# Kernel tuning notes

Measured on AMD Instinct MI355X. Metric: run time of the kernel, lower is better.

## Reference

```python
import jax, jax.numpy as jnp
import numpy as np

N = 50000      # nodes
E = 800000     # edges (before self loops)
D_IN = 64      # input atom feature dim
HID = 128      # hidden_dim
HEADS = 4
C = HID // HEADS  # 32 per-head channels
ED = 12        # edge feature dim
L = 4          # num GAT layers
EPS = 1e-5


def setup_inputs() -> dict:
    key = jax.random.key(0)
    ks = jax.random.split(key, 10)
    s = 0.1
    return {
        "x": jax.random.normal(ks[0], (N, D_IN), jnp.float32),
        "edge_index": jax.random.randint(ks[1], (2, E), 0, N, dtype=jnp.int32),
        "edge_attr": jax.random.uniform(ks[2], (E, ED), jnp.float32),
        "Wp": jax.random.normal(ks[3], (D_IN, HID), jnp.float32) * s,
        "bp": jnp.zeros((HID,), jnp.float32),
        "W": jax.random.normal(ks[4], (L, HID, HID), jnp.float32) * s,
        "We": jax.random.normal(ks[5], (L, ED, HID), jnp.float32) * s,
        "att_src": jax.random.normal(ks[6], (L, HEADS, C), jnp.float32) * s,
        "att_dst": jax.random.normal(ks[7], (L, HEADS, C), jnp.float32) * s,
        "att_edge": jax.random.normal(ks[8], (L, HEADS, C), jnp.float32) * s,
        "bias": jnp.zeros((L, HID), jnp.float32),
        "gamma": jnp.ones((L, HID), jnp.float32),
        "beta": jnp.zeros((L, HID), jnp.float32),
    }


def _gat_layer(h, src, dst, ea_full, W, We, a_s, a_d, a_e, b):
    # PyG GATConv: x' = x W -> [N, heads, C]; attention uses edge features, msg = alpha * x'_src
    xp = (h @ W).reshape(N, HEADS, C)
    e_emb = (ea_full @ We).reshape(-1, HEADS, C)          # [E', heads, C]
    a_src = (xp * a_s).sum(-1)                            # [N, heads]
    a_dst = (xp * a_d).sum(-1)
    a = a_src[src] + a_dst[dst] + (e_emb * a_e).sum(-1)   # [E', heads]
    a = jax.nn.leaky_relu(a, 0.2)
    # segment softmax over destination node neighborhoods
    amax = jax.ops.segment_max(a, dst, num_segments=N)
    ex = jnp.exp(a - amax[dst])
    denom = jax.ops.segment_sum(ex, dst, num_segments=N)
    alpha = ex / denom[dst]                               # [E', heads]
    msg = alpha[:, :, None] * xp[src]                     # [E', heads, C]
    out = jax.ops.segment_sum(msg, dst, num_segments=N)   # [N, heads, C]
    return out.reshape(N, HID) + b


def reference(x, edge_index, edge_attr, Wp, bp, W, We, att_src, att_dst, att_edge, bias, gamma, beta):
    # PyG GATConv add_self_loops=True with fill_value='mean' for edge_attr
    loop = jnp.arange(N, dtype=edge_index.dtype)
    src = jnp.concatenate([edge_index[0], loop])
    dst = jnp.concatenate([edge_index[1], loop])
    ea_mean = edge_attr.mean(0)
    ea_full = jnp.concatenate([edge_attr, jnp.broadcast_to(ea_mean, (N, ED))], 0)

    h = jax.nn.relu(x @ Wp + bp)
    for i in range(L):
        h_in = h
        h = _gat_layer(h, src, dst, ea_full, W[i], We[i], att_src[i], att_dst[i], att_edge[i], bias[i])
        # BatchNorm1d (training-mode batch statistics)
        mu = h.mean(0)
        var = ((h - mu) ** 2).mean(0)
        h = gamma[i] * (h - mu) / jnp.sqrt(var + EPS) + beta[i]
        h = jax.nn.relu(h)
        if i > 0:
            h = h + h_in
    return h
```

## Files before the change

kernel.cpp:

```cpp
#include <hip/hip_runtime.h>

constexpr int N_NODES = 50000;
constexpr int N_EDGES = 800000;
constexpr int N_ETOT  = N_EDGES + N_NODES;
constexpr int HID     = 128;
constexpr int HEADS   = 4;
constexpr int ED      = 12;
constexpr int LAYERS  = 4;
constexpr float BN_EPS = 1e-5f;
constexpr int SCAN_BLK = (N_NODES + 255) / 256;
constexpr int EB = (N_ETOT + 255) / 256;
constexpr int GB = (N_NODES + 63) / 64;
constexpr int WB = (LAYERS * HID * HID + 255) / 256;

typedef __attribute__((ext_vector_type(8))) short short8;
typedef __attribute__((ext_vector_type(4))) float floatx4;

__device__ inline unsigned bf16pair(float a, float b) {
    unsigned ua = __float_as_uint(a), ub = __float_as_uint(b);
    ua = (ua + 0x7FFFu + ((ua >> 16) & 1u)) >> 16;
    ub = (ub + 0x7FFFu + ((ub >> 16) & 1u)) >> 16;
    return ua | (ub << 16);
}

__launch_bounds__(256)
__global__ void pre1_kernel(const int* __restrict__ dst, int* __restrict__ hist,
                            int* __restrict__ rank,
                            const float* __restrict__ ea, float* __restrict__ easum,
                            const float* __restrict__ W, unsigned short* __restrict__ wb) {
    __shared__ float ls[12];
    int bid = blockIdx.x, t = threadIdx.x;
    if (bid < EB) {
        int e = bid * 256 + t;
        if (e < N_ETOT) {
            int d = (e < N_EDGES) ? dst[e] : (e - N_EDGES);
            rank[e] = atomicAdd(&hist[d], 1);
        }
    } else if (bid < EB + 256) {
        int b2 = bid - EB;
        if (t < 12) ls[t] = 0.f;
        __syncthreads();
        float loc[12];
#pragma unroll
        for (int d = 0; d < 12; d++) loc[d] = 0.f;
        for (int e = b2 * 256 + t; e < N_EDGES; e += 256 * 256) {
            const float* er = ea + (size_t)e * ED;
#pragma unroll
            for (int d = 0; d < 12; d++) loc[d] += er[d];
        }
#pragma unroll
        for (int d = 0; d < 12; d++) atomicAdd(&ls[d], loc[d]);
        __syncthreads();
        if (t < 12) atomicAdd(&easum[t], ls[t]);
    } else {
        int idx = (bid - EB - 256) * 256 + t;
        if (idx < LAYERS * HID * HID) {
            int l = idx >> 14;
            int k = (idx >> 7) & 127;
            int n = idx & 127;
            unsigned u = __float_as_uint(W[idx]);
            u = (u + 0x7FFFu + ((u >> 16) & 1u)) >> 16;
            int kt = k >> 5, q = (k & 31) >> 3, j = k & 7;
            int nt = n >> 4, c = n & 15;
            int lane = q * 16 + c;
            wb[(size_t)l * 16384 + ((size_t)(kt * 8 + nt) * 64 + lane) * 8 + j] =
                (unsigned short)u;
        }
    }
}

__global__ void blocksum_kernel(const int* __restrict__ hist, int* __restrict__ bsum) {
    __shared__ int sd[256];
    int t = threadIdx.x;
    int n = blockIdx.x * 256 + t;
    sd[t] = (n < N_NODES) ? hist[n] : 0;
    __syncthreads();
#pragma unroll
    for (int off = 128; off; off >>= 1) {
        if (t < off) sd[t] += sd[t + off];
        __syncthreads();
    }
    if (t == 0) bsum[blockIdx.x] = sd[0];
}

__launch_bounds__(256)
__global__ void pre2_kernel(const int* __restrict__ bsum, int* __restrict__ boff,
                            int* __restrict__ rowp, const float* __restrict__ easum,
                            const float* __restrict__ We, const float* __restrict__ att_edge,
                            float* __restrict__ wea_all, float* __restrict__ aloop) {
    int t = threadIdx.x;
    if (blockIdx.x == 0) {
        __shared__ int sd[256];
        int v = (t < SCAN_BLK) ? bsum[t] : 0;
        sd[t] = v;
        __syncthreads();
#pragma unroll
        for (int off = 1; off < 256; off <<= 1) {
            int u = (t >= off) ? sd[t - off] : 0;
            __syncthreads();
            sd[t] += u;
            __syncthreads();
        }
        if (t < SCAN_BLK) boff[t] = sd[t] - v;
        if (t == 255) rowp[N_NODES] = sd[255];
    } else {
        __shared__ float em[12];
        __shared__ float weash[LAYERS * ED * HEADS];
        if (t < 12) em[t] = easum[t] / (float)N_EDGES;
        if (t < LAYERS * ED * HEADS) {
            int l = t / (ED * HEADS);
            int r = t % (ED * HEADS);
            int d = r / HEADS;
            int h = r % HEADS;
            float sum = 0.f;
#pragma unroll
            for (int c = 0; c < 32; c++)
                sum += We[((size_t)(l * ED + d)) * HID + h * 32 + c] *
                       att_edge[(l * HEADS + h) * 32 + c];
            wea_all[t] = sum;
            weash[t] = sum;
        }
        __syncthreads();
        if (t < LAYERS * HEADS) {
            int l = t / HEADS, h = t % HEADS;
            float s = 0.f;
#pragma unroll
            for (int d = 0; d < 12; d++) s += em[d] * weash[l * ED * HEADS + d * HEADS + h];
            aloop[t] = s;
        }
    }
}

__global__ void rowp_kernel(const int* __restrict__ hist, const int* __restrict__ boff,
                            int* __restrict__ rowp) {
    __shared__ int sd[256];
    int t = threadIdx.x;
    int n = blockIdx.x * 256 + t;
    int v = (n < N_NODES) ? hist[n] : 0;
    sd[t] = v;
    __syncthreads();
#pragma unroll
    for (int off = 1; off < 256; off <<= 1) {
        int u = (t >= off) ? sd[t - off] : 0;
        __syncthreads();
        sd[t] += u;
        __syncthreads();
    }
    if (n < N_NODES) {
        int excl = sd[t] - v + boff[blockIdx.x];
        rowp[n] = excl;
    }
}

__launch_bounds__(256)
__global__ void pre3_kernel(const int* __restrict__ src, const int* __restrict__ dst,
                            const int* __restrict__ rank, const int* __restrict__ rowp,
                            int2* __restrict__ csr,
                            const float* __restrict__ A, const float* __restrict__ B,
                            const float* __restrict__ bias, float* __restrict__ C,
                            unsigned* __restrict__ Cb) {
    __shared__ float Bs[64 * 128];
    int t = threadIdx.x;
    if (blockIdx.x < EB) {
        int e = blockIdx.x * 256 + t;
        if (e >= N_ETOT) return;
        int s, d;
        if (e < N_EDGES) { s = src[e]; d = dst[e]; }
        else             { s = d = e - N_EDGES; }
        int pos = rowp[d] + rank[e];
        csr[pos] = make_int2(s, e);
        return;
    }
    constexpr int K = 64;
    int bid = blockIdx.x - EB;
    const float4* B4 = (const float4*)B;
    float4* Bs4 = (float4*)Bs;
#pragma unroll
    for (int i = t; i < K * 32; i += 256) Bs4[i] = B4[i];
    __syncthreads();

    int c0 = (t & 15) * 8;
    int r0 = (t >> 4) * 4;
    int rbase = bid * 64 + r0;

    float acc[4][8];
#pragma unroll
    for (int j = 0; j < 4; j++)
#pragma unroll
        for (int c = 0; c < 8; c++) acc[j][c] = 0.f;

    const float4* A4 = (const float4*)A;
    int rg[4];
#pragma unroll
    for (int j = 0; j < 4; j++) rg[j] = min(rbase + j, N_NODES - 1);

    for (int kk = 0; kk < K; kk += 4) {
        float4 av[4];
#pragma unroll
        for (int j = 0; j < 4; j++) av[j] = A4[(size_t)rg[j] * (K / 4) + (kk >> 2)];
        float a_arr[4][4];
#pragma unroll
        for (int j = 0; j < 4; j++) {
            a_arr[j][0] = av[j].x; a_arr[j][1] = av[j].y;
            a_arr[j][2] = av[j].z; a_arr[j][3] = av[j].w;
        }
#pragma unroll
        for (int jj = 0; jj < 4; jj++) {
            float4 b0 = Bs4[(kk + jj) * 32 + (c0 >> 2)];
            float4 b1 = Bs4[(kk + jj) * 32 + (c0 >> 2) + 1];
#pragma unroll
            for (int j = 0; j < 4; j++) {
                float a = a_arr[j][jj];
                acc[j][0] += a * b0.x; acc[j][1] += a * b0.y;
                acc[j][2] += a * b0.z; acc[j][3] += a * b0.w;
                acc[j][4] += a * b1.x; acc[j][5] += a * b1.y;
                acc[j][6] += a * b1.z; acc[j][7] += a * b1.w;
            }
        }
    }

#pragma unroll
    for (int j = 0; j < 4; j++) {
        int r = rbase + j;
        if (r < N_NODES) {
            float o[8];
#pragma unroll
            for (int c = 0; c < 8; c++) o[c] = fmaxf(acc[j][c] + bias[c0 + c], 0.f);
            ((float4*)(C + (size_t)r * 128 + c0))[0] = make_float4(o[0], o[1], o[2], o[3]);
            ((float4*)(C + (size_t)r * 128 + c0 + 4))[0] = make_float4(o[4], o[5], o[6], o[7]);
            uint4 pk;
            pk.x = bf16pair(o[0], o[1]); pk.y = bf16pair(o[2], o[3]);
            pk.z = bf16pair(o[4], o[5]); pk.w = bf16pair(o[6], o[7]);
            ((uint4*)(Cb + (size_t)r * 64 + (c0 >> 1)))[0] = pk;
        }
    }
}

__launch_bounds__(256)
__global__ void pre4_kernel(const int2* __restrict__ csr, const float* __restrict__ ea,
                            const float* __restrict__ wea_all, const float* __restrict__ aloop,
                            uint2* __restrict__ aecsr,
                            const unsigned short* __restrict__ hAb,
                            const unsigned short* __restrict__ wb,
                            const float* __restrict__ att_s, const float* __restrict__ att_d,
                            unsigned* __restrict__ xpb,
                            float* __restrict__ asrc, float* __restrict__ adst) {
    __shared__ float smem[4 * 16 * 129];
    int t = threadIdx.x;
    if (blockIdx.x < EB) {
        float* wsh = smem;
        float* lsh = smem + 192;
        if (t < LAYERS * ED * HEADS) wsh[t] = wea_all[t];
        if (t < LAYERS * HEADS) lsh[t] = aloop[t];
        __syncthreads();
        int i = blockIdx.x * 256 + t;
        if (i >= N_ETOT) return;
        int e = csr[i].y;
        float a[LAYERS][4];
        if (e < N_EDGES) {
            float er[12];
            const float* ep = ea + (size_t)e * ED;
#pragma unroll
            for (int d = 0; d < 12; d++) er[d] = ep[d];
#pragma unroll
            for (int l = 0; l < LAYERS; l++)
#pragma unroll
                for (int h = 0; h < 4; h++) {
                    float s = 0.f;
#pragma unroll
                    for (int d = 0; d < 12; d++) s += er[d] * wsh[l * 48 + d * 4 + h];
                    a[l][h] = s;
                }
        } else {
#pragma unroll
            for (int l = 0; l < LAYERS; l++)
#pragma unroll
                for (int h = 0; h < 4; h++) a[l][h] = lsh[l * 4 + h];
        }
#pragma unroll
        for (int l = 0; l < LAYERS; l++)
            aecsr[(size_t)l * N_ETOT + i] =
                make_uint2(bf16pair(a[l][0], a[l][1]), bf16pair(a[l][2], a[l][3]));
        return;
    }
    int bid = blockIdx.x - EB;
    float (*lds)[16][129] = (float (*)[16][129])smem;
    int w = t >> 6, lane = t & 63;
    int rbase = bid * 64 + w * 16;
    int mrow = lane & 15, quad = lane >> 4;

    floatx4 acc[8];
#pragma unroll
    for (int nt = 0; nt < 8; nt++) acc[nt] = (floatx4){0.f, 0.f, 0.f, 0.f};

    int arow = min(rbase + mrow, N_NODES - 1);
    const short8* wb8 = (const short8*)wb;
#pragma unroll
    for (int kt = 0; kt < 4; kt++) {
        short8 afrag = *(const short8*)(hAb + (size_t)arow * 128 + kt * 32 + quad * 8);
#pragma unroll
        for (int nt = 0; nt < 8; nt++) {
            short8 bfrag = wb8[(kt * 8 + nt) * 64 + lane];
            acc[nt] = __builtin_amdgcn_mfma_f32_16x16x32_bf16(afrag, bfrag, acc[nt], 0, 0, 0);
        }
    }
#pragma unroll
    for (int nt = 0; nt < 8; nt++)
#pragma unroll
        for (int rr = 0; rr < 4; rr++)
            lds[w][quad * 4 + rr][nt * 16 + mrow] = acc[nt][rr];

    int row = lane >> 2, h = lane & 3;
    int r = rbase + row;
    float vals[32];
    float ps = 0.f, pd = 0.f;
#pragma unroll
    for (int c = 0; c < 32; c++) {
        float v = lds[w][row][h * 32 + c];
        vals[c] = v;
        ps += v * att_s[h * 32 + c];
        pd += v * att_d[h * 32 + c];
    }
    if (r < N_NODES) {
        unsigned* dstp = xpb + (size_t)r * 64 + h * 16;
#pragma unroll
        for (int qq = 0; qq < 4; qq++) {
            uint4 o;
            o.x = bf16pair(vals[qq * 8 + 0], vals[qq * 8 + 1]);
            o.y = bf16pair(vals[qq * 8 + 2], vals[qq * 8 + 3]);
            o.z = bf16pair(vals[qq * 8 + 4], vals[qq * 8 + 5]);
            o.w = bf16pair(vals[qq * 8 + 6], vals[qq * 8 + 7]);
            ((uint4*)dstp)[qq] = o;
        }
        asrc[r * 4 + h] = ps;
        adst[r * 4 + h] = pd;
    }
}

template <int ADD>
__launch_bounds__(256)
__global__ void gemm_fused_kernel(const float* __restrict__ outb,
                                  const float* __restrict__ bnsum,
                                  const float* __restrict__ bnsum2,
                                  const float* __restrict__ gamma,
                                  const float* __restrict__ beta,
                                  float* __restrict__ hA,
                                  const unsigned short* __restrict__ wb,
                                  const float* __restrict__ att_s,
                                  const float* __restrict__ att_d,
                                  unsigned* __restrict__ xpb,
                                  float* __restrict__ asrc, float* __restrict__ adst) {
    __shared__ float lds[4][16][129];
    __shared__ float sc_s[128], sh_s[128];
    int t = threadIdx.x;
    if (t < 128) {
        float mu = bnsum[t] / (float)N_NODES;
        float var = bnsum2[t] / (float)N_NODES - mu * mu;
        float inv = rsqrtf(var + BN_EPS);
        float g = gamma[t] * inv;
        sc_s[t] = g;
        sh_s[t] = beta[t] - mu * g;
    }
    __syncthreads();

    int w = t >> 6, lane = t & 63;
    int rbase = blockIdx.x * 64 + w * 16;
    int mrow = lane & 15, quad = lane >> 4;
    int arow = rbase + mrow;
    bool owner = arow < N_NODES;
    int ar = min(arow, N_NODES - 1);

    floatx4 acc[8];
#pragma unroll
    for (int nt = 0; nt < 8; nt++) acc[nt] = (floatx4){0.f, 0.f, 0.f, 0.f};

    const short8* wb8 = (const short8*)wb;
#pragma unroll
    for (int kt = 0; kt < 4; kt++) {
        int cb = kt * 32 + quad * 8;
        const float4* ob = (const float4*)(outb + (size_t)ar * 128 + cb);
        float4 o0 = ob[0], o1 = ob[1];
        float v[8];
        v[0] = fmaxf(o0.x * sc_s[cb + 0] + sh_s[cb + 0], 0.f);
        v[1] = fmaxf(o0.y * sc_s[cb + 1] + sh_s[cb + 1], 0.f);
        v[2] = fmaxf(o0.z * sc_s[cb + 2] + sh_s[cb + 2], 0.f);
        v[3] = fmaxf(o0.w * sc_s[cb + 3] + sh_s[cb + 3], 0.f);
        v[4] = fmaxf(o1.x * sc_s[cb + 4] + sh_s[cb + 4], 0.f);
        v[5] = fmaxf(o1.y * sc_s[cb + 5] + sh_s[cb + 5], 0.f);
        v[6] = fmaxf(o1.z * sc_s[cb + 6] + sh_s[cb + 6], 0.f);
        v[7] = fmaxf(o1.w * sc_s[cb + 7] + sh_s[cb + 7], 0.f);
        if (ADD) {
            const float4* hp = (const float4*)(hA + (size_t)ar * 128 + cb);
            float4 h0 = hp[0], h1 = hp[1];
            v[0] += h0.x; v[1] += h0.y; v[2] += h0.z; v[3] += h0.w;
            v[4] += h1.x; v[5] += h1.y; v[6] += h1.z; v[7] += h1.w;
        }
        if (owner) {
            float4* hw = (float4*)(hA + (size_t)ar * 128 + cb);
            hw[0] = make_float4(v[0], v[1], v[2], v[3]);
            hw[1] = make_float4(v[4], v[5], v[6], v[7]);
        }
        uint4 pk;
        pk.x = bf16pair(v[0], v[1]); pk.y = bf16pair(v[2], v[3]);
        pk.z = bf16pair(v[4], v[5]); pk.w = bf16pair(v[6], v[7]);
        short8 afrag = *(short8*)&pk;
#pragma unroll
        for (int nt = 0; nt < 8; nt++) {
            short8 bfrag = wb8[(kt * 8 + nt) * 64 + lane];
            acc[nt] = __builtin_amdgcn_mfma_f32_16x16x32_bf16(afrag, bfrag, acc[nt], 0, 0, 0);
        }
    }

#pragma unroll
    for (int nt = 0; nt < 8; nt++)
#pragma unroll
        for (int rr = 0; rr < 4; rr++)
            lds[w][quad * 4 + rr][nt * 16 + mrow] = acc[nt][rr];

    int row = lane >> 2, h = lane & 3;
    int r = rbase + row;
    float vals[32];
    float ps = 0.f, pd = 0.f;
#pragma unroll
    for (int c = 0; c < 32; c++) {
        float v = lds[w][row][h * 32 + c];
        vals[c] = v;
        ps += v * att_s[h * 32 + c];
        pd += v * att_d[h * 32 + c];
    }
    if (r < N_NODES) {
        unsigned* dstp = xpb + (size_t)r * 64 + h * 16;
#pragma unroll
        for (int qq = 0; qq < 4; qq++) {
            uint4 o;
            o.x = bf16pair(vals[qq * 8 + 0], vals[qq * 8 + 1]);
            o.y = bf16pair(vals[qq * 8 + 2], vals[qq * 8 + 3]);
            o.z = bf16pair(vals[qq * 8 + 4], vals[qq * 8 + 5]);
            o.w = bf16pair(vals[qq * 8 + 6], vals[qq * 8 + 7]);
            ((uint4*)dstp)[qq] = o;
        }
        asrc[r * 4 + h] = ps;
        adst[r * 4 + h] = pd;
    }
}

__launch_bounds__(256)
__global__ void node_kernel(const uint2* __restrict__ aecsr, const float* __restrict__ asrc,
                            const float* __restrict__ adst, const int* __restrict__ rowp,
                            const int2* __restrict__ csr, const unsigned* __restrict__ xpb,
                            float* __restrict__ out) {
    int gw = (blockIdx.x * blockDim.x + threadIdx.x) >> 6;
    int lane = threadIdx.x & 63;
    if (gw >= N_NODES) return;
    int sub = lane >> 4;
    int sl  = lane & 15;
    int h   = sl >> 2;
    int beg = rowp[gw], end = rowp[gw + 1];
    const uint4* xp4 = (const uint4*)xpb;
    float adh = adst[gw * 4 + h];

    float a[8];
#pragma unroll
    for (int c = 0; c < 8; c++) a[c] = 0.f;
    float den = 0.f;

#define PROC(JJ)                                                                 \
    {                                                                            \
        int2 se = csr[JJ];                                                       \
        uint2 ae = aecsr[JJ];                                                    \
        unsigned aw = (h & 2) ? ae.y : ae.x;                                     \
        float aeh = __uint_as_float((h & 1) ? (aw & 0xFFFF0000u) : (aw << 16));  \
        float ash = asrc[se.x * 4 + h];                                          \
        uint4 v = xp4[(size_t)se.x * 16 + sl];                                   \
        float lg = ash + adh + aeh;                                              \
        lg = (lg > 0.f) ? lg : 0.2f * lg;                                        \
        float ex = __expf(fminf(lg, 60.f));                                      \
        a[0] += ex * __uint_as_float(v.x << 16);                                 \
        a[1] += ex * __uint_as_float(v.x & 0xFFFF0000u);                         \
        a[2] += ex * __uint_as_float(v.y << 16);                                 \
        a[3] += ex * __uint_as_float(v.y & 0xFFFF0000u);                         \
        a[4] += ex * __uint_as_float(v.z << 16);                                 \
        a[5] += ex * __uint_as_float(v.z & 0xFFFF0000u);                         \
        a[6] += ex * __uint_as_float(v.w << 16);                                 \
        a[7] += ex * __uint_as_float(v.w & 0xFFFF0000u);                         \
        den += ex;                                                               \
    }

    int j = beg + sub;
    for (; j + 12 < end; j += 16) {
        PROC(j); PROC(j + 4); PROC(j + 8); PROC(j + 12);
    }
    for (; j < end; j += 4) PROC(j);
#undef PROC

#pragma unroll
    for (int c = 0; c < 8; c++) {
        a[c] += __shfl_xor(a[c], 16);
        a[c] += __shfl_xor(a[c], 32);
    }
    den += __shfl_xor(den, 16);
    den += __shfl_xor(den, 32);
    float inv = 1.0f / den;
    if (sub == 0) {
        float* op = out + (size_t)gw * 128 + sl * 8;
        ((float4*)op)[0] = make_float4(a[0] * inv, a[1] * inv, a[2] * inv, a[3] * inv);
        ((float4*)op)[1] = make_float4(a[4] * inv, a[5] * inv, a[6] * inv, a[7] * inv);
    }
}

__launch_bounds__(256)
__global__ void bnstats_kernel(const float* __restrict__ h, float* __restrict__ bnsum,
                               float* __restrict__ bnsum2) {
    __shared__ float ls[256], ls2[256];
    int t = threadIdx.x;
    int c = t & 127, half = t >> 7;
    int r0 = blockIdx.x * 128;
    float s = 0.f, s2 = 0.f;
    int rend = min(r0 + 128, N_NODES);
    for (int r = r0 + half; r < rend; r += 2) {
        float v = h[(size_t)r * 128 + c];
        s += v; s2 += v * v;
    }
    ls[t] = s; ls2[t] = s2;
    __syncthreads();
    if (half == 0) {
        s += ls[t + 128]; s2 += ls2[t + 128];
        atomicAdd(&bnsum[c], s);
        atomicAdd(&bnsum2[c], s2);
    }
}

__launch_bounds__(256)
__global__ void finalupd_kernel(const float* __restrict__ outb, const float* __restrict__ bnsum,
                                const float* __restrict__ bnsum2, const float* __restrict__ gamma,
                                const float* __restrict__ beta, const float* __restrict__ hA,
                                float* __restrict__ dst) {
    __shared__ float sc_s[128], sh_s[128];
    int t = threadIdx.x;
    if (t < 128) {
        float mu = bnsum[t] / (float)N_NODES;
        float var = bnsum2[t] / (float)N_NODES - mu * mu;
        float inv = rsqrtf(var + BN_EPS);
        float g = gamma[t] * inv;
        sc_s[t] = g;
        sh_s[t] = beta[t] - mu * g;
    }
    __syncthreads();
    int i = blockIdx.x * blockDim.x + t;
    if (i >= N_NODES * 32) return;
    int c4 = (i & 31) * 4;
    float4 o = ((const float4*)outb)[i];
    float4 hh = ((const float4*)hA)[i];
    float4 v;
    v.x = fmaxf(o.x * sc_s[c4 + 0] + sh_s[c4 + 0], 0.f) + hh.x;
    v.y = fmaxf(o.y * sc_s[c4 + 1] + sh_s[c4 + 1], 0.f) + hh.y;
    v.z = fmaxf(o.z * sc_s[c4 + 2] + sh_s[c4 + 2], 0.f) + hh.z;
    v.w = fmaxf(o.w * sc_s[c4 + 3] + sh_s[c4 + 3], 0.f) + hh.w;
    ((float4*)dst)[i] = v;
}

extern "C" void kernel_launch(void* const* d_in, const int* in_sizes, int n_in,
                              void* d_out, int out_size, void* d_ws, size_t ws_size,
                              hipStream_t stream) {
    const float* x          = (const float*)d_in[0];
    const int*   edge_index = (const int*)d_in[1];
    const float* edge_attr  = (const float*)d_in[2];
    const float* Wp         = (const float*)d_in[3];
    const float* bp         = (const float*)d_in[4];
    const float* W          = (const float*)d_in[5];
    const float* We         = (const float*)d_in[6];
    const float* att_src    = (const float*)d_in[7];
    const float* att_dst    = (const float*)d_in[8];
    const float* att_edge   = (const float*)d_in[9];
    const float* gamma      = (const float*)d_in[11];
    const float* beta       = (const float*)d_in[12];
    float* outp = (float*)d_out;

    const int* ei_src = edge_index;
    const int* ei_dst = edge_index + N_EDGES;

    char* p = (char*)d_ws;
    auto alloc = [&](size_t nbytes) {
        char* r = p;
        p += (nbytes + 255) & ~(size_t)255;
        return r;
    };
    int*   hist     = (int*)alloc((size_t)N_NODES * 4);
    float* easum    = (float*)alloc(16 * 4);
    float* bnsumall = (float*)alloc((size_t)LAYERS * 256 * 4);
    size_t zero_bytes = (char*)(bnsumall + LAYERS * 256) - (char*)hist;

    float* hA       = (float*)alloc((size_t)N_NODES * 128 * 4);
    unsigned* hAb   = (unsigned*)alloc((size_t)N_NODES * 64 * 4);
    unsigned* xpb   = (unsigned*)alloc((size_t)N_NODES * 64 * 4);
    float* outb     = (float*)alloc((size_t)N_NODES * 128 * 4);
    float* asrc     = (float*)alloc((size_t)N_NODES * 4 * 4);
    float* adst     = (float*)alloc((size_t)N_NODES * 4 * 4);
    float* wea_all  = (float*)alloc((LAYERS * 48 + 16) * 4);
    float* aloop    = wea_all + LAYERS * 48;
    unsigned short* wb = (unsigned short*)alloc((size_t)LAYERS * 16384 * 2);
    int* rowp       = (int*)alloc(((size_t)N_NODES + 1) * 4);
    int* rankbuf    = (int*)alloc((size_t)N_ETOT * 4);
    int2* csr       = (int2*)alloc((size_t)N_ETOT * 8);
    uint2* aecsr    = (uint2*)alloc((size_t)LAYERS * N_ETOT * 8);
    int* bsum       = (int*)alloc(256 * 4);
    int* boff       = (int*)alloc(256 * 4);

    (void)hipMemsetAsync(hist, 0, zero_bytes, stream);

    pre1_kernel<<<EB + 256 + WB, 256, 0, stream>>>(ei_dst, hist, rankbuf, edge_attr, easum, W, wb);
    blocksum_kernel<<<SCAN_BLK, 256, 0, stream>>>(hist, bsum);
    pre2_kernel<<<2, 256, 0, stream>>>(bsum, boff, rowp, easum, We, att_edge, wea_all, aloop);
    rowp_kernel<<<SCAN_BLK, 256, 0, stream>>>(hist, boff, rowp);
    pre3_kernel<<<EB + GB, 256, 0, stream>>>(ei_src, ei_dst, rankbuf, rowp, csr, x, Wp, bp, hA, hAb);
    pre4_kernel<<<EB + GB, 256, 0, stream>>>(csr, edge_attr, wea_all, aloop, aecsr,
                                             (const unsigned short*)hAb, wb,
                                             att_src, att_dst, xpb, asrc, adst);

    for (int l = 0; l < LAYERS; l++) {
        float* bnsum  = bnsumall + l * 256;
        float* bnsum2 = bnsum + 128;
        node_kernel<<<(N_NODES + 3) / 4, 256, 0, stream>>>(
            aecsr + (size_t)l * N_ETOT, asrc, adst, rowp, csr, xpb, outb);
        bnstats_kernel<<<(N_NODES + 127) / 128, 256, 0, stream>>>(outb, bnsum, bnsum2);
        if (l < LAYERS - 1) {
            if (l == 0)
                gemm_fused_kernel<0><<<GB, 256, 0, stream>>>(
                    outb, bnsum, bnsum2, gamma + l * 128, beta + l * 128, hA,
                    wb + (size_t)(l + 1) * 16384, att_src + (l + 1) * 128,
                    att_dst + (l + 1) * 128, xpb, asrc, adst);
            else
                gemm_fused_kernel<1><<<GB, 256, 0, stream>>>(
                    outb, bnsum, bnsum2, gamma + l * 128, beta + l * 128, hA,
                    wb + (size_t)(l + 1) * 16384, att_src + (l + 1) * 128,
                    att_dst + (l + 1) * 128, xpb, asrc, adst);
        } else {
            finalupd_kernel<<<(N_NODES * 32 + 255) / 256, 256, 0, stream>>>(
                outb, bnsum, bnsum2, gamma + l * 128, beta + l * 128, hA, outp);
        }
    }
}
```

Before: 615.7 us.

## Replicate degree histogram to cut atomic contention and regroup preprocessing kernels

```diff
diff --git a/kernel.cpp b/kernel.cpp
--- a/kernel.cpp
+++ b/kernel.cpp
@@ -8,7 +8,9 @@
 constexpr int ED      = 12;
 constexpr int LAYERS  = 4;
 constexpr float BN_EPS = 1e-5f;
-constexpr int SCAN_BLK = (N_NODES + 255) / 256;
+constexpr int R_REP = 4;
+constexpr int RN = N_NODES * R_REP;
+constexpr int SB2 = (RN + 255) / 256;
 constexpr int EB = (N_ETOT + 255) / 256;
 constexpr int GB = (N_NODES + 63) / 64;
 constexpr int WB = (LAYERS * HID * HID + 255) / 256;
@@ -24,20 +26,87 @@
 }
 
 __launch_bounds__(256)
-__global__ void pre1_kernel(const int* __restrict__ dst, int* __restrict__ hist,
+__global__ void pre1_kernel(const int* __restrict__ dst, int* __restrict__ hist2,
                             int* __restrict__ rank,
                             const float* __restrict__ ea, float* __restrict__ easum,
-                            const float* __restrict__ W, unsigned short* __restrict__ wb) {
-    __shared__ float ls[12];
+                            const float* __restrict__ W, unsigned short* __restrict__ wb,
+                            const float* __restrict__ A, const float* __restrict__ B,
+                            const float* __restrict__ bias, float* __restrict__ C,
+                            unsigned* __restrict__ Cb) {
+    __shared__ float smem[64 * 128];
     int bid = blockIdx.x, t = threadIdx.x;
-    if (bid < EB) {
-        int e = bid * 256 + t;
+    if (bid < GB) {
+        constexpr int K = 64;
+        const float4* B4 = (const float4*)B;
+        float4* Bs4 = (float4*)smem;
+#pragma unroll
+        for (int i = t; i < K * 32; i += 256) Bs4[i] = B4[i];
+        __syncthreads();
+
+        int c0 = (t & 15) * 8;
+        int r0 = (t >> 4) * 4;
+        int rbase = bid * 64 + r0;
+
+        float acc[4][8];
+#pragma unroll
+        for (int j = 0; j < 4; j++)
+#pragma unroll
+            for (int c = 0; c < 8; c++) acc[j][c] = 0.f;
+
+        const float4* A4 = (const float4*)A;
+        int rg[4];
+#pragma unroll
+        for (int j = 0; j < 4; j++) rg[j] = min(rbase + j, N_NODES - 1);
+
+        for (int kk = 0; kk < K; kk += 4) {
+            float4 av[4];
+#pragma unroll
+            for (int j = 0; j < 4; j++) av[j] = A4[(size_t)rg[j] * (K / 4) + (kk >> 2)];
+            float a_arr[4][4];
+#pragma unroll
+            for (int j = 0; j < 4; j++) {
+                a_arr[j][0] = av[j].x; a_arr[j][1] = av[j].y;
+                a_arr[j][2] = av[j].z; a_arr[j][3] = av[j].w;
+            }
+#pragma unroll
+            for (int jj = 0; jj < 4; jj++) {
+                float4 b0 = Bs4[(kk + jj) * 32 + (c0 >> 2)];
+                float4 b1 = Bs4[(kk + jj) * 32 + (c0 >> 2) + 1];
+#pragma unroll
+                for (int j = 0; j < 4; j++) {
+                    float a = a_arr[j][jj];
+                    acc[j][0] += a * b0.x; acc[j][1] += a * b0.y;
+                    acc[j][2] += a * b0.z; acc[j][3] += a * b0.w;
+                    acc[j][4] += a * b1.x; acc[j][5] += a * b1.y;
+                    acc[j][6] += a * b1.z; acc[j][7] += a * b1.w;
+                }
+            }
+        }
+
+#pragma unroll
+        for (int j = 0; j < 4; j++) {
+            int r = rbase + j;
+            if (r < N_NODES) {
+                float o[8];
+#pragma unroll
+                for (int c = 0; c < 8; c++) o[c] = fmaxf(acc[j][c] + bias[c0 + c], 0.f);
+                ((float4*)(C + (size_t)r * 128 + c0))[0] = make_float4(o[0], o[1], o[2], o[3]);
+                ((float4*)(C + (size_t)r * 128 + c0 + 4))[0] = make_float4(o[4], o[5], o[6], o[7]);
+                uint4 pk;
+                pk.x = bf16pair(o[0], o[1]); pk.y = bf16pair(o[2], o[3]);
+                pk.z = bf16pair(o[4], o[5]); pk.w = bf16pair(o[6], o[7]);
+                ((uint4*)(Cb + (size_t)r * 64 + (c0 >> 1)))[0] = pk;
+            }
+        }
+    } else if (bid < GB + EB) {
+        int e = (bid - GB) * 256 + t;
         if (e < N_ETOT) {
             int d = (e < N_EDGES) ? dst[e] : (e - N_EDGES);
-            rank[e] = atomicAdd(&hist[d], 1);
-        }
-    } else if (bid < EB + 256) {
-        int b2 = bid - EB;
+            rank[e] = atomicAdd(&hist2[(e & (R_REP - 1)) * N_NODES + d], 1);
+        }
+    } else if (bid < GB + EB + 256) {
+        int b2 = bid - GB - EB;
+        float* ls = smem;
         if (t < 12) ls[t] = 0.f;
         __syncthreads();
         float loc[12];
@@ -53,7 +122,7 @@
         __syncthreads();
         if (t < 12) atomicAdd(&easum[t], ls[t]);
     } else {
-        int idx = (bid - EB - 256) * 256 + t;
+        int idx = (bid - GB - EB - 256) * 256 + t;
         if (idx < LAYERS * HID * HID) {
             int l = idx >> 14;
             int k = (idx >> 7) & 127;
@@ -69,11 +138,13 @@
     }
 }
 
-__global__ void blocksum_kernel(const int* __restrict__ hist, int* __restrict__ bsum) {
+__global__ void blocksum_kernel(const int* __restrict__ hist2, int* __restrict__ bsum) {
     __shared__ int sd[256];
     int t = threadIdx.x;
-    int n = blockIdx.x * 256 + t;
-    sd[t] = (n < N_NODES) ? hist[n] : 0;
+    int f = blockIdx.x * 256 + t;
+    int v = 0;
+    if (f < RN) v = hist2[(f & (R_REP - 1)) * N_NODES + (f >> 2)];
+    sd[t] = v;
     __syncthreads();
 #pragma unroll
     for (int off = 128; off; off >>= 1) {
@@ -85,14 +156,19 @@
 
 __launch_bounds__(256)
 __global__ void pre2_kernel(const int* __restrict__ bsum, int* __restrict__ boff,
-                            int* __restrict__ rowp, const float* __restrict__ easum,
+                            int* __restrict__ rowpR, const float* __restrict__ easum,
                             const float* __restrict__ We, const float* __restrict__ att_edge,
                             float* __restrict__ wea_all, float* __restrict__ aloop) {
     int t = threadIdx.x;
     if (blockIdx.x == 0) {
         __shared__ int sd[256];
-        int v = (t < SCAN_BLK) ? bsum[t] : 0;
-        sd[t] = v;
+        int b = 4 * t;
+        int v0 = (b + 0 < SB2) ? bsum[b + 0] : 0;
+        int v1 = (b + 1 < SB2) ? bsum[b + 1] : 0;
+        int v2 = (b + 2 < SB2) ? bsum[b + 2] : 0;
+        int v3 = (b + 3 < SB2) ? bsum[b + 3] : 0;
+        int tot = v0 + v1 + v2 + v3;
+        sd[t] = tot;
         __syncthreads();
 #pragma unroll
         for (int off = 1; off < 256; off <<= 1) {
@@ -101,8 +177,12 @@
             sd[t] += u;
             __syncthreads();
         }
-        if (t < SCAN_BLK) boff[t] = sd[t] - v;
-        if (t == 255) rowp[N_NODES] = sd[255];
+        int excl = sd[t] - tot;
+        if (b + 0 < SB2) boff[b + 0] = excl;
+        if (b + 1 < SB2) boff[b + 1] = excl + v0;
+        if (b + 2 < SB2) boff[b + 2] = excl + v0 + v1;
+        if (b + 3 < SB2) boff[b + 3] = excl + v0 + v1 + v2;
+        if (t == 255) rowpR[RN] = sd[255];
     } else {
         __shared__ float em[12];
         __shared__ float weash[LAYERS * ED * HEADS];
@@ -131,12 +211,12 @@
     }
 }
 
-__global__ void rowp_kernel(const int* __restrict__ hist, const int* __restrict__ boff,
-                            int* __restrict__ rowp) {
+__global__ void rowp_kernel(const int* __restrict__ hist2, const int* __restrict__ boff,
+                            int* __restrict__ rowpR) {
     __shared__ int sd[256];
     int t = threadIdx.x;
-    int n = blockIdx.x * 256 + t;
-    int v = (n < N_NODES) ? hist[n] : 0;
+    int f = blockIdx.x * 256 + t;
+    int v = (f < RN) ? hist2[(f & (R_REP - 1)) * N_NODES + (f >> 2)] : 0;
     sd[t] = v;
     __syncthreads();
 #pragma unroll
@@ -146,144 +226,31 @@
         sd[t] += u;
         __syncthreads();
     }
-    if (n < N_NODES) {
-        int excl = sd[t] - v + boff[blockIdx.x];
-        rowp[n] = excl;
-    }
-}
-
-__launch_bounds__(256)
-__global__ void pre3_kernel(const int* __restrict__ src, const int* __restrict__ dst,
-                            const int* __restrict__ rank, const int* __restrict__ rowp,
-                            int2* __restrict__ csr,
-                            const float* __restrict__ A, const float* __restrict__ B,
-                            const float* __restrict__ bias, float* __restrict__ C,
-                            unsigned* __restrict__ Cb) {
-    __shared__ float Bs[64 * 128];
-    int t = threadIdx.x;
-    if (blockIdx.x < EB) {
-        int e = blockIdx.x * 256 + t;
+    if (f < RN) rowpR[f] = sd[t] - v + boff[blockIdx.x];
+}
+
+__launch_bounds__(256)
+__global__ void pre3_kernel(const unsigned short* __restrict__ hAb,
+                            const unsigned short* __restrict__ wb,
+                            const float* __restrict__ att_s, const float* __restrict__ att_d,
+                            unsigned* __restrict__ xpb,
+                            float* __restrict__ asrc, float* __restrict__ adst,
+                            const int* __restrict__ src, const int* __restrict__ dst,
+                            const int* __restrict__ rank, const int* __restrict__ rowpR,
+                            int2* __restrict__ csr) {
+    __shared__ float smem[4 * 16 * 129];
+    int t = threadIdx.x;
+    if (blockIdx.x >= GB) {
+        int e = (blockIdx.x - GB) * 256 + t;
         if (e >= N_ETOT) return;
         int s, d;
         if (e < N_EDGES) { s = src[e]; d = dst[e]; }
         else             { s = d = e - N_EDGES; }
-        int pos = rowp[d] + rank[e];
+        int pos = rowpR[d * R_REP + (e & (R_REP - 1))] + rank[e];
         csr[pos] = make_int2(s, e);
         return;
     }
-    constexpr int K = 64;
-    int bid = blockIdx.x - EB;
-    const float4* B4 = (const float4*)B;
-    float4* Bs4 = (float4*)Bs;
-#pragma unroll
-    for (int i = t; i < K * 32; i += 256) Bs4[i] = B4[i];
-    __syncthreads();
-
-    int c0 = (t & 15) * 8;
-    int r0 = (t >> 4) * 4;
-    int rbase = bid * 64 + r0;
-
-    float acc[4][8];
-#pragma unroll
-    for (int j = 0; j < 4; j++)
-#pragma unroll
-        for (int c = 0; c < 8; c++) acc[j][c] = 0.f;
-
-    const float4* A4 = (const float4*)A;
-    int rg[4];
-#pragma unroll
-    for (int j = 0; j < 4; j++) rg[j] = min(rbase + j, N_NODES - 1);
-
-    for (int kk = 0; kk < K; kk += 4) {
-        float4 av[4];
-#pragma unroll
-        for (int j = 0; j < 4; j++) av[j] = A4[(size_t)rg[j] * (K / 4) + (kk >> 2)];
-        float a_arr[4][4];
-#pragma unroll
-        for (int j = 0; j < 4; j++) {
-            a_arr[j][0] = av[j].x; a_arr[j][1] = av[j].y;
-            a_arr[j][2] = av[j].z; a_arr[j][3] = av[j].w;
-        }
-#pragma unroll
-        for (int jj = 0; jj < 4; jj++) {
-            float4 b0 = Bs4[(kk + jj) * 32 + (c0 >> 2)];
-            float4 b1 = Bs4[(kk + jj) * 32 + (c0 >> 2) + 1];
-#pragma unroll
-            for (int j = 0; j < 4; j++) {
-                float a = a_arr[j][jj];
-                acc[j][0] += a * b0.x; acc[j][1] += a * b0.y;
-                acc[j][2] += a * b0.z; acc[j][3] += a * b0.w;
-                acc[j][4] += a * b1.x; acc[j][5] += a * b1.y;
-                acc[j][6] += a * b1.z; acc[j][7] += a * b1.w;
-            }
-        }
-    }
-
-#pragma unroll
-    for (int j = 0; j < 4; j++) {
-        int r = rbase + j;
-        if (r < N_NODES) {
-            float o[8];
-#pragma unroll
-            for (int c = 0; c < 8; c++) o[c] = fmaxf(acc[j][c] + bias[c0 + c], 0.f);
-            ((float4*)(C + (size_t)r * 128 + c0))[0] = make_float4(o[0], o[1], o[2], o[3]);
-            ((float4*)(C + (size_t)r * 128 + c0 + 4))[0] = make_float4(o[4], o[5], o[6], o[7]);
-            uint4 pk;
-            pk.x = bf16pair(o[0], o[1]); pk.y = bf16pair(o[2], o[3]);
-            pk.z = bf16pair(o[4], o[5]); pk.w = bf16pair(o[6], o[7]);
-            ((uint4*)(Cb + (size_t)r * 64 + (c0 >> 1)))[0] = pk;
-        }
-    }
-}
-
-__launch_bounds__(256)
-__global__ void pre4_kernel(const int2* __restrict__ csr, const float* __restrict__ ea,
-                            const float* __restrict__ wea_all, const float* __restrict__ aloop,
-                            uint2* __restrict__ aecsr,
-                            const unsigned short* __restrict__ hAb,
-                            const unsigned short* __restrict__ wb,
-                            const float* __restrict__ att_s, const float* __restrict__ att_d,
-                            unsigned* __restrict__ xpb,
-                            float* __restrict__ asrc, float* __restrict__ adst) {
-    __shared__ float smem[4 * 16 * 129];
-    int t = threadIdx.x;
-    if (blockIdx.x < EB) {
-        float* wsh = smem;
-        float* lsh = smem + 192;
-        if (t < LAYERS * ED * HEADS) wsh[t] = wea_all[t];
-        if (t < LAYERS * HEADS) lsh[t] = aloop[t];
-        __syncthreads();
-        int i = blockIdx.x * 256 + t;
-        if (i >= N_ETOT) return;
-        int e = csr[i].y;
-        float a[LAYERS][4];
-        if (e < N_EDGES) {
-            float er[12];
-            const float* ep = ea + (size_t)e * ED;
-#pragma unroll
-            for (int d = 0; d < 12; d++) er[d] = ep[d];
-#pragma unroll
-            for (int l = 0; l < LAYERS; l++)
-#pragma unroll
-                for (int h = 0; h < 4; h++) {
-                    float s = 0.f;
-#pragma unroll
-                    for (int d = 0; d < 12; d++) s += er[d] * wsh[l * 48 + d * 4 + h];
-                    a[l][h] = s;
-                }
-        } else {
-#pragma unroll
-            for (int l = 0; l < LAYERS; l++)
-#pragma unroll
-                for (int h = 0; h < 4; h++) a[l][h] = lsh[l * 4 + h];
-        }
-#pragma unroll
-        for (int l = 0; l < LAYERS; l++)
-            aecsr[(size_t)l * N_ETOT + i] =
-                make_uint2(bf16pair(a[l][0], a[l][1]), bf16pair(a[l][2], a[l][3]));
-        return;
-    }
-    int bid = blockIdx.x - EB;
+    int bid = blockIdx.x;
     float (*lds)[16][129] = (float (*)[16][129])smem;
     int w = t >> 6, lane = t & 63;
     int rbase = bid * 64 + w * 16;
@@ -335,6 +302,46 @@
         asrc[r * 4 + h] = ps;
         adst[r * 4 + h] = pd;
     }
+}
+
+__launch_bounds__(256)
+__global__ void pre4_kernel(const int2* __restrict__ csr, const float* __restrict__ ea,
+                            const float* __restrict__ wea_all, const float* __restrict__ aloop,
+                            uint2* __restrict__ aecsr) {
+    __shared__ float wsh[LAYERS * ED * HEADS];
+    __shared__ float lsh[LAYERS * HEADS];
+    int t = threadIdx.x;
+    if (t < LAYERS * ED * HEADS) wsh[t] = wea_all[t];
+    if (t < LAYERS * HEADS) lsh[t] = aloop[t];
+    __syncthreads();
+    int i = blockIdx.x * 256 + t;
+    if (i >= N_ETOT) return;
+    int e = csr[i].y;
+    float a[LAYERS][4];
+    if (e < N_EDGES) {
+        float er[12];
+        const float* ep = ea + (size_t)e * ED;
+#pragma unroll
+        for (int d = 0; d < 12; d++) er[d] = ep[d];
+#pragma unroll
+        for (int l = 0; l < LAYERS; l++)
+#pragma unroll
+            for (int h = 0; h < 4; h++) {
+                float s = 0.f;
+#pragma unroll
+                for (int d = 0; d < 12; d++) s += er[d] * wsh[l * 48 + d * 4 + h];
+                a[l][h] = s;
+            }
+    } else {
+#pragma unroll
+        for (int l = 0; l < LAYERS; l++)
+#pragma unroll
+            for (int h = 0; h < 4; h++) a[l][h] = lsh[l * 4 + h];
+    }
+#pragma unroll
+    for (int l = 0; l < LAYERS; l++)
+        aecsr[(size_t)l * N_ETOT + i] =
+            make_uint2(bf16pair(a[l][0], a[l][1]), bf16pair(a[l][2], a[l][3]));
 }
 
 template <int ADD>
@@ -446,7 +453,7 @@
 
 __launch_bounds__(256)
 __global__ void node_kernel(const uint2* __restrict__ aecsr, const float* __restrict__ asrc,
-                            const float* __restrict__ adst, const int* __restrict__ rowp,
+                            const float* __restrict__ adst, const int* __restrict__ rowpR,
                             const int2* __restrict__ csr, const unsigned* __restrict__ xpb,
                             float* __restrict__ out) {
     int gw = (blockIdx.x * blockDim.x + threadIdx.x) >> 6;
@@ -455,7 +462,7 @@
     int sub = lane >> 4;
     int sl  = lane & 15;
     int h   = sl >> 2;
-    int beg = rowp[gw], end = rowp[gw + 1];
+    int beg = rowpR[gw * R_REP], end = rowpR[(gw + 1) * R_REP];
     const uint4* xp4 = (const uint4*)xpb;
     float adh = adst[gw * 4 + h];
 
@@ -585,10 +592,10 @@
         p += (nbytes + 255) & ~(size_t)255;
         return r;
     };
-    int*   hist     = (int*)alloc((size_t)N_NODES * 4);
+    int*   hist2    = (int*)alloc((size_t)RN * 4);
     float* easum    = (float*)alloc(16 * 4);
     float* bnsumall = (float*)alloc((size_t)LAYERS * 256 * 4);
-    size_t zero_bytes = (char*)(bnsumall + LAYERS * 256) - (char*)hist;
+    size_t zero_bytes = (char*)(bnsumall + LAYERS * 256) - (char*)hist2;
 
     float* hA       = (float*)alloc((size_t)N_NODES * 128 * 4);
     unsigned* hAb   = (unsigned*)alloc((size_t)N_NODES * 64 * 4);
@@ -599,29 +606,30 @@
     float* wea_all  = (float*)alloc((LAYERS * 48 + 16) * 4);
     float* aloop    = wea_all + LAYERS * 48;
     unsigned short* wb = (unsigned short*)alloc((size_t)LAYERS * 16384 * 2);
-    int* rowp       = (int*)alloc(((size_t)N_NODES + 1) * 4);
+    int* rowpR      = (int*)alloc(((size_t)RN + 1) * 4);
     int* rankbuf    = (int*)alloc((size_t)N_ETOT * 4);
     int2* csr       = (int2*)alloc((size_t)N_ETOT * 8);
     uint2* aecsr    = (uint2*)alloc((size_t)LAYERS * N_ETOT * 8);
-    int* bsum       = (int*)alloc(256 * 4);
-    int* boff       = (int*)alloc(256 * 4);
-
-    (void)hipMemsetAsync(hist, 0, zero_bytes, stream);
-
-    pre1_kernel<<<EB + 256 + WB, 256, 0, stream>>>(ei_dst, hist, rankbuf, edge_attr, easum, W, wb);
-    blocksum_kernel<<<SCAN_BLK, 256, 0, stream>>>(hist, bsum);
-    pre2_kernel<<<2, 256, 0, stream>>>(bsum, boff, rowp, easum, We, att_edge, wea_all, aloop);
-    rowp_kernel<<<SCAN_BLK, 256, 0, stream>>>(hist, boff, rowp);
-    pre3_kernel<<<EB + GB, 256, 0, stream>>>(ei_src, ei_dst, rankbuf, rowp, csr, x, Wp, bp, hA, hAb);
-    pre4_kernel<<<EB + GB, 256, 0, stream>>>(csr, edge_attr, wea_all, aloop, aecsr,
-                                             (const unsigned short*)hAb, wb,
-                                             att_src, att_dst, xpb, asrc, adst);
+    int* bsum       = (int*)alloc(1024 * 4);
+    int* boff       = (int*)alloc(1024 * 4);
+
+    (void)hipMemsetAsync(hist2, 0, zero_bytes, stream);
+
+    pre1_kernel<<<GB + EB + 256 + WB, 256, 0, stream>>>(
+        ei_dst, hist2, rankbuf, edge_attr, easum, W, wb, x, Wp, bp, hA, hAb);
+    blocksum_kernel<<<SB2, 256, 0, stream>>>(hist2, bsum);
+    pre2_kernel<<<2, 256, 0, stream>>>(bsum, boff, rowpR, easum, We, att_edge, wea_all, aloop);
+    rowp_kernel<<<SB2, 256, 0, stream>>>(hist2, boff, rowpR);
+    pre3_kernel<<<GB + EB, 256, 0, stream>>>(
+        (const unsigned short*)hAb, wb, att_src, att_dst, xpb, asrc, adst,
+        ei_src, ei_dst, rankbuf, rowpR, csr);
+    pre4_kernel<<<EB, 256, 0, stream>>>(csr, edge_attr, wea_all, aloop, aecsr);
 
     for (int l = 0; l < LAYERS; l++) {
         float* bnsum  = bnsumall + l * 256;
         float* bnsum2 = bnsum + 128;
         node_kernel<<<(N_NODES + 3) / 4, 256, 0, stream>>>(
-            aecsr + (size_t)l * N_ETOT, asrc, adst, rowp, csr, xpb, outb);
+            aecsr + (size_t)l * N_ETOT, asrc, adst, rowpR, csr, xpb, outb);
         bnstats_kernel<<<(N_NODES + 127) / 128, 256, 0, stream>>>(outb, bnsum, bnsum2);
         if (l < LAYERS - 1) {
             if (l == 0)
```

Measured after the change: 597.5 us. -3.0%, faster.
